# Kernel optimization log

Measured on AMD Instinct MI355X. Metric: run time of the kernel, lower is better.

Reference implementation:

```python
import jax, jax.numpy as jnp
import numpy as np

N_NODES = 50000
N_EDGES = 800000
D_IN = 64
D_HID = 64
N_CLASSES = 10
N_GRAPHS = 128


def gcn_conv(x, src, dst, ew, W, b, n_nodes):
    """PyG-style GCNConv: add self-loops, symmetric degree normalization,
    linear transform, gather-scatter aggregation, bias."""
    loop = jnp.arange(n_nodes)
    src2 = jnp.concatenate([src, loop])
    dst2 = jnp.concatenate([dst, loop])
    ew2 = jnp.concatenate([ew, jnp.ones((n_nodes,), ew.dtype)])
    deg = jax.ops.segment_sum(ew2, dst2, num_segments=n_nodes)  # [N]
    dinv = jnp.where(deg > 0, jax.lax.rsqrt(deg), 0.0)
    norm = dinv[src2] * ew2 * dinv[dst2]                        # [E+N]
    xw = x @ W                                                  # [N, H]
    msg = xw[src2] * norm[:, None]                              # [E+N, H]
    out = jax.ops.segment_sum(msg, dst2, num_segments=n_nodes)  # [N, H]
    return out + b


def setup_inputs() -> dict:
    key = jax.random.key(0)
    ks = jax.random.split(key, 10)
    x = jax.random.normal(ks[0], (N_NODES, D_IN), dtype=jnp.float32)
    edge_index = jax.random.randint(ks[1], (2, N_EDGES), 0, N_NODES, dtype=jnp.int64)
    batch = jnp.sort(jax.random.randint(ks[2], (N_NODES,), 0, N_GRAPHS, dtype=jnp.int64))
    edge_weights = jax.random.uniform(ks[3], (N_EDGES,), dtype=jnp.float32)
    s = 1.0 / np.sqrt(D_HID)
    W1 = jax.random.normal(ks[4], (D_IN, D_HID), dtype=jnp.float32) * s
    W2 = jax.random.normal(ks[5], (D_HID, D_HID), dtype=jnp.float32) * s
    W3 = jax.random.normal(ks[6], (D_HID, D_HID), dtype=jnp.float32) * s
    W_lin = jax.random.normal(ks[7], (D_HID, N_CLASSES), dtype=jnp.float32) * s
    return {
        "x": x, "edge_index": edge_index, "batch": batch, "edge_weights": edge_weights,
        "W1": W1, "b1": jnp.zeros((D_HID,), jnp.float32),
        "W2": W2, "b2": jnp.zeros((D_HID,), jnp.float32),
        "W3": W3, "b3": jnp.zeros((D_HID,), jnp.float32),
        "W_lin": W_lin, "b_lin": jnp.zeros((N_CLASSES,), jnp.float32),
    }


def reference(x, edge_index, batch, edge_weights, W1, b1, W2, b2, W3, b3, W_lin, b_lin):
    n_nodes = x.shape[0]
    src, dst = edge_index[0], edge_index[1]
    h1 = jax.nn.relu(gcn_conv(x, src, dst, edge_weights, W1, b1, n_nodes))
    h2 = jax.nn.relu(gcn_conv(h1, src, dst, edge_weights, W2, b2, n_nodes))
    h3 = gcn_conv(h2, src, dst, edge_weights, W3, b3, n_nodes)  # embedding: no relu
    # global_mean_pool over graphs in the batch
    sums = jax.ops.segment_sum(h3, batch, num_segments=N_GRAPHS)           # [G, H]
    cnt = jax.ops.segment_sum(jnp.ones((n_nodes,), h3.dtype), batch, num_segments=N_GRAPHS)
    pooled = sums / jnp.maximum(cnt, 1.0)[:, None]
    return pooled @ W_lin + b_lin  # [G, C]
```

## Files before the change

kernel.cpp:

```cpp
#include <hip/hip_runtime.h>
#include <hip/hip_fp16.h>

#define N_NODES   50000
#define N_EDGES   800000
#define D         64
#define N_CLASSES 10
#define N_GRAPHS  128
#define ELLW      48
#define CPAD      16
#define NXCD      8
#define DPART     (N_NODES / NXCD)


__device__ __forceinline__ float unpack_ew(int p) {
    return __half2float(__ushort_as_half((unsigned short)((unsigned)p >> 16)));
}


__global__ __launch_bounds__(256) void ell_scatter(const int* __restrict__ src,
                                                   const int* __restrict__ dst,
                                                   const float* __restrict__ ew,
                                                   int* __restrict__ count,
                                                   unsigned int* __restrict__ ell) {
    const int grp = blockIdx.x & (NXCD - 1);
    const int ord = blockIdx.x >> 3;
    const int lo  = grp * DPART;
#pragma unroll
    for (int i = 0; i < 8; ++i) {
        int e = ord * 2048 + i * 256 + threadIdx.x;
        if (e < N_EDGES) {
            int d = dst[e];
            if ((unsigned)(d - lo) < (unsigned)DPART) {
                int s = src[e];
                float w = ew[e];
                int c = atomicAdd(&count[d * CPAD], 1);
                if (c < ELLW) {
                    ell[d * ELLW + c] = (unsigned int)s |
                        ((unsigned int)__half_as_ushort(__float2half_rn(w)) << 16);
                }
            }
        }
    }
}

__global__ __launch_bounds__(256) void node_dinv(const int* __restrict__ count,
                                                 const unsigned int* __restrict__ ell,
                                                 float* __restrict__ dinv) {
    const int lane = threadIdx.x & 63;
    const int gwave = (blockIdx.x * blockDim.x + threadIdx.x) >> 6;
    const int nw = (gridDim.x * blockDim.x) >> 6;
    for (int i = gwave; i < N_NODES; i += nw) {
        int cnt = min(count[i * CPAD], ELLW);
        float w = (lane < cnt) ? unpack_ew((int)ell[i * ELLW + lane]) : 0.0f;
#pragma unroll
        for (int off = 32; off >= 1; off >>= 1) w += __shfl_xor(w, off);
        if (lane == 0) dinv[i] = rsqrtf(1.0f + w);
    }
}


__device__ __forceinline__ void gather_pair(const int* __restrict__ count,
                                            const unsigned int* __restrict__ ell,
                                            const __half* __restrict__ xwh,
                                            int rowA, int rowB, int lane,
                                            float& accA, float& accB) {
    int cntA = min(count[rowA * CPAD], ELLW);
    int cntB = min(count[rowB * CPAD], ELLW);
    const int4* mA = (const int4*)(ell + (size_t)rowA * ELLW);
    const int4* mB = (const int4*)(ell + (size_t)rowB * ELLW);
    accA = __half2float(xwh[(size_t)rowA * D + lane]);
    accB = __half2float(xwh[(size_t)rowB * D + lane]);
    int cm = max(cntA, cntB);
    for (int j = 0; j < cm; j += 8) {
        int4 a0 = mA[j / 4 + 0];
        int4 a1 = mA[j / 4 + 1];
        int4 b0 = mB[j / 4 + 0];
        int4 b1 = mB[j / 4 + 1];
        int pA[8] = {a0.x, a0.y, a0.z, a0.w, a1.x, a1.y, a1.z, a1.w};
        int pB[8] = {b0.x, b0.y, b0.z, b0.w, b1.x, b1.y, b1.z, b1.w};
#pragma unroll
        for (int t = 0; t < 8; ++t) pA[t] = (j + t < cntA) ? pA[t] : 0;
#pragma unroll
        for (int t = 0; t < 8; ++t) pB[t] = (j + t < cntB) ? pB[t] : 0;
        float vA[8], vB[8];
#pragma unroll
        for (int t = 0; t < 8; ++t)
            vA[t] = __half2float(xwh[(size_t)(pA[t] & 0xFFFF) * D + lane]);
#pragma unroll
        for (int t = 0; t < 8; ++t)
            vB[t] = __half2float(xwh[(size_t)(pB[t] & 0xFFFF) * D + lane]);
#pragma unroll
        for (int t = 0; t < 8; ++t) accA = fmaf(vA[t], unpack_ew(pA[t]), accA);
#pragma unroll
        for (int t = 0; t < 8; ++t) accB = fmaf(vB[t], unpack_ew(pB[t]), accB);
    }
}


__global__ __launch_bounds__(256) void gemm_rows(const float* __restrict__ in,
                                                 const float* __restrict__ W,
                                                 const float* __restrict__ dinv,
                                                 __half* __restrict__ xwh) {
    __shared__ float  Wl[D * D];
    __shared__ float4 xq[4][64];
    for (int i = threadIdx.x; i < D * D; i += blockDim.x) Wl[i] = W[i];
    __syncthreads();

    const int lane = threadIdx.x & 63;
    const int wid  = threadIdx.x >> 6;
    float w[D];
#pragma unroll
    for (int k = 0; k < D; ++k) w[k] = Wl[k * D + lane];

    const int q = (blockIdx.x * blockDim.x + threadIdx.x) >> 6;
    const int r0 = q * 4;

    xq[wid][lane] = ((const float4*)(in + (size_t)r0 * D))[lane];
    float dv0 = dinv[r0 + 0], dv1 = dinv[r0 + 1];
    float dv2 = dinv[r0 + 2], dv3 = dinv[r0 + 3];
    const float4* xr = (const float4*)xq[wid];
    float acc0 = 0.0f, acc1 = 0.0f, acc2 = 0.0f, acc3 = 0.0f;
#pragma unroll
    for (int k4 = 0; k4 < D / 4; ++k4) {
        float4 x0 = xr[0 * 16 + k4];
        float4 x1 = xr[1 * 16 + k4];
        float4 x2 = xr[2 * 16 + k4];
        float4 x3 = xr[3 * 16 + k4];
        float w0 = w[4 * k4 + 0], w1 = w[4 * k4 + 1];
        float w2 = w[4 * k4 + 2], w3 = w[4 * k4 + 3];
        acc0 = fmaf(x0.x, w0, acc0); acc0 = fmaf(x0.y, w1, acc0);
        acc0 = fmaf(x0.z, w2, acc0); acc0 = fmaf(x0.w, w3, acc0);
        acc1 = fmaf(x1.x, w0, acc1); acc1 = fmaf(x1.y, w1, acc1);
        acc1 = fmaf(x1.z, w2, acc1); acc1 = fmaf(x1.w, w3, acc1);
        acc2 = fmaf(x2.x, w0, acc2); acc2 = fmaf(x2.y, w1, acc2);
        acc2 = fmaf(x2.z, w2, acc2); acc2 = fmaf(x2.w, w3, acc2);
        acc3 = fmaf(x3.x, w0, acc3); acc3 = fmaf(x3.y, w1, acc3);
        acc3 = fmaf(x3.z, w2, acc3); acc3 = fmaf(x3.w, w3, acc3);
    }
    xwh[(size_t)(r0 + 0) * D + lane] = __float2half(acc0 * dv0);
    xwh[(size_t)(r0 + 1) * D + lane] = __float2half(acc1 * dv1);
    xwh[(size_t)(r0 + 2) * D + lane] = __float2half(acc2 * dv2);
    xwh[(size_t)(r0 + 3) * D + lane] = __float2half(acc3 * dv3);
}

__global__ __launch_bounds__(256) void aggemm(const int* __restrict__ count,
                                              const unsigned int* __restrict__ ell,
                                              const float* __restrict__ dinv,
                                              const __half* __restrict__ xin,
                                              const float* __restrict__ bias,
                                              const float* __restrict__ W,
                                              __half* __restrict__ xout) {
    __shared__ float Wl[D * D];
    __shared__ float rb[4][2][D];
    for (int i = threadIdx.x; i < D * D; i += blockDim.x) Wl[i] = W[i];
    __syncthreads();

    const int lane = threadIdx.x & 63;
    const int wid  = threadIdx.x >> 6;
    const int q = __builtin_amdgcn_readfirstlane(
        (blockIdx.x * blockDim.x + threadIdx.x) >> 6);
    const float bv = bias[lane];

    int rowA = 2 * q, rowB = 2 * q + 1;
    float accA, accB;
    gather_pair(count, ell, xin, rowA, rowB, lane, accA, accB);
    float dvA = dinv[rowA], dvB = dinv[rowB];
    float sA = fmaxf(fmaf(accA, dvA, bv), 0.0f);
    float sB = fmaxf(fmaf(accB, dvB, bv), 0.0f);
    rb[wid][0][lane] = sA;
    rb[wid][1][lane] = sB;
    const float4* rA4 = (const float4*)rb[wid][0];
    const float4* rB4 = (const float4*)rb[wid][1];
    float oA = 0.0f, oB = 0.0f;
#pragma unroll
    for (int k4 = 0; k4 < D / 4; ++k4) {
        float4 ra = rA4[k4];
        float4 rbv = rB4[k4];
        float w0 = Wl[(4 * k4 + 0) * D + lane];
        float w1 = Wl[(4 * k4 + 1) * D + lane];
        float w2 = Wl[(4 * k4 + 2) * D + lane];
        float w3 = Wl[(4 * k4 + 3) * D + lane];
        oA = fmaf(ra.x, w0, oA);  oB = fmaf(rbv.x, w0, oB);
        oA = fmaf(ra.y, w1, oA);  oB = fmaf(rbv.y, w1, oB);
        oA = fmaf(ra.z, w2, oA);  oB = fmaf(rbv.z, w2, oB);
        oA = fmaf(ra.w, w3, oA);  oB = fmaf(rbv.w, w3, oB);
    }
    xout[(size_t)rowA * D + lane] = __float2half(oA * dvA);
    xout[(size_t)rowB * D + lane] = __float2half(oB * dvB);
}

__global__ __launch_bounds__(256) void node_agg(const int* __restrict__ count,
                                                const unsigned int* __restrict__ ell,
                                                const float* __restrict__ dinv,
                                                const __half* __restrict__ xwh,
                                                const float* __restrict__ bias,
                                                float* __restrict__ agg) {
    const int lane = threadIdx.x & 63;
    const int q = __builtin_amdgcn_readfirstlane(
        (blockIdx.x * blockDim.x + threadIdx.x) >> 6);
    const float bv = bias[lane];

    int rowA = 2 * q, rowB = 2 * q + 1;
    float accA, accB;
    gather_pair(count, ell, xwh, rowA, rowB, lane, accA, accB);
    agg[(size_t)rowA * D + lane] = fmaf(accA, dinv[rowA], bv);
    agg[(size_t)rowB * D + lane] = fmaf(accB, dinv[rowB], bv);
}


__global__ __launch_bounds__(256) void pool(const float* __restrict__ agg3,
                                            const int* __restrict__ batch,
                                            float* __restrict__ pooled,
                                            float* __restrict__ cnt) {
    const int lane = threadIdx.x & 63;
    const int gwave = (blockIdx.x * blockDim.x + threadIdx.x) >> 6;
    const int nw = (gridDim.x * blockDim.x) >> 6;
    const int chunk = (N_NODES + nw - 1) / nw;
    int r0 = gwave * chunk;
    int r1 = min(r0 + chunk, N_NODES);
    if (r0 >= r1) return;

    int g = batch[r0];
    float acc = 0.0f;
    int c = 0;
    for (int row = r0; row < r1; ++row) {
        int gg = batch[row];
        if (gg != g) {
            atomicAdd(&pooled[g * D + lane], acc);
            if (lane == 0) atomicAdd(&cnt[g], (float)c);
            g = gg; acc = 0.0f; c = 0;
        }
        acc += agg3[(size_t)row * D + lane];
        ++c;
    }
    atomicAdd(&pooled[g * D + lane], acc);
    if (lane == 0) atomicAdd(&cnt[g], (float)c);
}

__global__ __launch_bounds__(64) void final_lin(const float* __restrict__ pooled,
                                                const float* __restrict__ cnt,
                                                const float* __restrict__ Wlin,
                                                const float* __restrict__ blin,
                                                float* __restrict__ out) {
    __shared__ float row[D];
    int g = blockIdx.x;
    int t = threadIdx.x;
    float c = fmaxf(cnt[g], 1.0f);
    row[t] = pooled[g * D + t] / c;
    __syncthreads();
    if (t < N_CLASSES) {
        float acc = blin[t];
#pragma unroll
        for (int k = 0; k < D; ++k) acc = fmaf(row[k], Wlin[k * N_CLASSES + t], acc);
        out[g * N_CLASSES + t] = acc;
    }
}


extern "C" void kernel_launch(void* const* d_in, const int* in_sizes, int n_in,
                              void* d_out, int out_size, void* d_ws, size_t ws_size,
                              hipStream_t stream) {
    const float* x     = (const float*)d_in[0];
    const int*   ei    = (const int*)d_in[1];
    const int*   src   = ei;
    const int*   dst   = ei + N_EDGES;
    const int*   batch = (const int*)d_in[2];
    const float* ew    = (const float*)d_in[3];
    const float* W1    = (const float*)d_in[4];
    const float* b1    = (const float*)d_in[5];
    const float* W2    = (const float*)d_in[6];
    const float* b2    = (const float*)d_in[7];
    const float* W3    = (const float*)d_in[8];
    const float* b3    = (const float*)d_in[9];
    const float* Wlin  = (const float*)d_in[10];
    const float* blin  = (const float*)d_in[11];
    float* out = (float*)d_out;

    float*        ws     = (float*)d_ws;
    __half*       xwhA   = (__half*)ws;
    __half*       xwhB   = (__half*)(ws + 1600000);
    float*        agg3   = ws + 3200000;
    unsigned int* ell    = (unsigned int*)(ws + 6400000);
    float*        dinv   = ws + 8800000;
    int*          count  = (int*)(ws + 8850000);
    float*        pooled = ws + 9650000;
    float*        cnt    = ws + 9658192;

    const int B = 256;

    (void)hipMemsetAsync(count, 0, N_NODES * CPAD * sizeof(int), stream);
    (void)hipMemsetAsync(pooled, 0, (N_GRAPHS * D + N_GRAPHS) * sizeof(float), stream);

    const int pairBlocks = 6250;
    const int quadBlocks = 3125;

    ell_scatter<<<391 * NXCD, B, 0, stream>>>(src, dst, ew, count, ell);
    node_dinv<<<3125, B, 0, stream>>>(count, ell, dinv);

    gemm_rows<<<quadBlocks, B, 0, stream>>>(x, W1, dinv, xwhA);
    aggemm<<<pairBlocks, B, 0, stream>>>(count, ell, dinv, xwhA, b1, W2, xwhB);
    aggemm<<<pairBlocks, B, 0, stream>>>(count, ell, dinv, xwhB, b2, W3, xwhA);
    node_agg<<<pairBlocks, B, 0, stream>>>(count, ell, dinv, xwhA, b3, agg3);

    pool<<<196, B, 0, stream>>>(agg3, batch, pooled, cnt);
    final_lin<<<N_GRAPHS, 64, 0, stream>>>(pooled, cnt, Wlin, blin, out);
}
```

Measured before the change: 262.8 us.

## Split wave into half-waves gathering two rows with half2 loads

The gather kernels now give each 32-lane half of a wave one destination row, with each lane loading a packed pair of fp16 features as a single 32-bit load. Previously every lane loaded one fp16 value for both rows, so each wave issued 16 scattered 2-byte loads per 8 neighbours. Now it issues 8 wider loads, halving the gather instruction count and widening the per-lane access. The fused GEMM and the output stores use float2/half2 accordingly. The cost is a per-lane select between the two rows' neighbour lists and divergent loop trip counts across the two halves.

```diff
diff --git a/kernel.cpp b/kernel.cpp
--- a/kernel.cpp
+++ b/kernel.cpp
@@ -14,6 +14,12 @@
 
 __device__ __forceinline__ float unpack_ew(int p) {
     return __half2float(__ushort_as_half((unsigned short)((unsigned)p >> 16)));
+}
+__device__ __forceinline__ float h_lo(unsigned v) {
+    return __half2float(__ushort_as_half((unsigned short)(v & 0xFFFF)));
+}
+__device__ __forceinline__ float h_hi(unsigned v) {
+    return __half2float(__ushort_as_half((unsigned short)(v >> 16)));
 }
 
 
@@ -59,17 +65,20 @@
 }
 
 
-__device__ __forceinline__ void gather_pair(const int* __restrict__ count,
-                                            const unsigned int* __restrict__ ell,
-                                            const __half* __restrict__ xwh,
-                                            int rowA, int rowB, int lane,
-                                            float& accA, float& accB) {
+__device__ __forceinline__ void gather_h2(const int* __restrict__ count,
+                                          const unsigned int* __restrict__ ell,
+                                          const __half* __restrict__ xwh,
+                                          int q, int sub, int hf,
+                                          float& alo, float& ahi) {
+    const int rowA = 2 * q, rowB = 2 * q + 1;
     int cntA = min(count[rowA * CPAD], ELLW);
     int cntB = min(count[rowB * CPAD], ELLW);
     const int4* mA = (const int4*)(ell + (size_t)rowA * ELLW);
     const int4* mB = (const int4*)(ell + (size_t)rowB * ELLW);
-    accA = __half2float(xwh[(size_t)rowA * D + lane]);
-    accB = __half2float(xwh[(size_t)rowB * D + lane]);
+    const int rowh = rowA + hf;
+    unsigned sv = *(const unsigned*)(xwh + (size_t)rowh * D + 2 * sub);
+    alo = h_lo(sv);
+    ahi = h_hi(sv);
     int cm = max(cntA, cntB);
     for (int j = 0; j < cm; j += 8) {
         int4 a0 = mA[j / 4 + 0];
@@ -82,17 +91,19 @@
         for (int t = 0; t < 8; ++t) pA[t] = (j + t < cntA) ? pA[t] : 0;
 #pragma unroll
         for (int t = 0; t < 8; ++t) pB[t] = (j + t < cntB) ? pB[t] : 0;
-        float vA[8], vB[8];
+        int ps[8];
+#pragma unroll
+        for (int t = 0; t < 8; ++t) ps[t] = hf ? pB[t] : pA[t];
+        unsigned vv[8];
 #pragma unroll
         for (int t = 0; t < 8; ++t)
-            vA[t] = __half2float(xwh[(size_t)(pA[t] & 0xFFFF) * D + lane]);
-#pragma unroll
-        for (int t = 0; t < 8; ++t)
-            vB[t] = __half2float(xwh[(size_t)(pB[t] & 0xFFFF) * D + lane]);
-#pragma unroll
-        for (int t = 0; t < 8; ++t) accA = fmaf(vA[t], unpack_ew(pA[t]), accA);
-#pragma unroll
-        for (int t = 0; t < 8; ++t) accB = fmaf(vB[t], unpack_ew(pB[t]), accB);
+            vv[t] = *(const unsigned*)(xwh + (size_t)(ps[t] & 0xFFFF) * D + 2 * sub);
+#pragma unroll
+        for (int t = 0; t < 8; ++t) {
+            float w = unpack_ew(ps[t]);
+            alo = fmaf(h_lo(vv[t]), w, alo);
+            ahi = fmaf(h_hi(vv[t]), w, ahi);
+        }
     }
 }
 
@@ -156,37 +167,34 @@
     __syncthreads();
 
     const int lane = threadIdx.x & 63;
+    const int sub  = lane & 31;
+    const int hf   = lane >> 5;
     const int wid  = threadIdx.x >> 6;
     const int q = __builtin_amdgcn_readfirstlane(
         (blockIdx.x * blockDim.x + threadIdx.x) >> 6);
-    const float bv = bias[lane];
-
-    int rowA = 2 * q, rowB = 2 * q + 1;
-    float accA, accB;
-    gather_pair(count, ell, xin, rowA, rowB, lane, accA, accB);
-    float dvA = dinv[rowA], dvB = dinv[rowB];
-    float sA = fmaxf(fmaf(accA, dvA, bv), 0.0f);
-    float sB = fmaxf(fmaf(accB, dvB, bv), 0.0f);
-    rb[wid][0][lane] = sA;
-    rb[wid][1][lane] = sB;
-    const float4* rA4 = (const float4*)rb[wid][0];
-    const float4* rB4 = (const float4*)rb[wid][1];
-    float oA = 0.0f, oB = 0.0f;
+    const float2 bv = *(const float2*)&bias[2 * sub];
+
+    const int rowh = 2 * q + hf;
+    float alo, ahi;
+    gather_h2(count, ell, xin, q, sub, hf, alo, ahi);
+    float dv = dinv[rowh];
+    float s0 = fmaxf(fmaf(alo, dv, bv.x), 0.0f);
+    float s1 = fmaxf(fmaf(ahi, dv, bv.y), 0.0f);
+    *(float2*)&rb[wid][hf][2 * sub] = make_float2(s0, s1);
+    const float4* r4 = (const float4*)rb[wid][hf];
+    float o0 = 0.0f, o1 = 0.0f;
 #pragma unroll
     for (int k4 = 0; k4 < D / 4; ++k4) {
-        float4 ra = rA4[k4];
-        float4 rbv = rB4[k4];
-        float w0 = Wl[(4 * k4 + 0) * D + lane];
-        float w1 = Wl[(4 * k4 + 1) * D + lane];
-        float w2 = Wl[(4 * k4 + 2) * D + lane];
-        float w3 = Wl[(4 * k4 + 3) * D + lane];
-        oA = fmaf(ra.x, w0, oA);  oB = fmaf(rbv.x, w0, oB);
-        oA = fmaf(ra.y, w1, oA);  oB = fmaf(rbv.y, w1, oB);
-        oA = fmaf(ra.z, w2, oA);  oB = fmaf(rbv.z, w2, oB);
-        oA = fmaf(ra.w, w3, oA);  oB = fmaf(rbv.w, w3, oB);
-    }
-    xout[(size_t)rowA * D + lane] = __float2half(oA * dvA);
-    xout[(size_t)rowB * D + lane] = __float2half(oB * dvB);
+        float4 r = r4[k4];
+#pragma unroll
+        for (int i = 0; i < 4; ++i) {
+            float rk = (i == 0) ? r.x : (i == 1) ? r.y : (i == 2) ? r.z : r.w;
+            float2 wv = *(const float2*)&Wl[(4 * k4 + i) * D + 2 * sub];
+            o0 = fmaf(rk, wv.x, o0);
+            o1 = fmaf(rk, wv.y, o1);
+        }
+    }
+    *(__half2*)(xout + (size_t)rowh * D + 2 * sub) = __floats2half2_rn(o0 * dv, o1 * dv);
 }
 
 __global__ __launch_bounds__(256) void node_agg(const int* __restrict__ count,
@@ -196,15 +204,18 @@
                                                 const float* __restrict__ bias,
                                                 float* __restrict__ agg) {
     const int lane = threadIdx.x & 63;
+    const int sub  = lane & 31;
+    const int hf   = lane >> 5;
     const int q = __builtin_amdgcn_readfirstlane(
         (blockIdx.x * blockDim.x + threadIdx.x) >> 6);
-    const float bv = bias[lane];
-
-    int rowA = 2 * q, rowB = 2 * q + 1;
-    float accA, accB;
-    gather_pair(count, ell, xwh, rowA, rowB, lane, accA, accB);
-    agg[(size_t)rowA * D + lane] = fmaf(accA, dinv[rowA], bv);
-    agg[(size_t)rowB * D + lane] = fmaf(accB, dinv[rowB], bv);
+    const float2 bv = *(const float2*)&bias[2 * sub];
+
+    const int rowh = 2 * q + hf;
+    float alo, ahi;
+    gather_h2(count, ell, xwh, q, sub, hf, alo, ahi);
+    float dv = dinv[rowh];
+    *(float2*)(agg + (size_t)rowh * D + 2 * sub) =
+        make_float2(fmaf(alo, dv, bv.x), fmaf(ahi, dv, bv.y));
 }
 
 
```

Result: slower. 270.4 us (+2.9%).
